# Optimization experiments

Measured on AMD Instinct MI355X. Metric: run time of the kernel, lower is better.

The kernel has to match this reference:

```python
import jax, jax.numpy as jnp
import numpy as np

SEQ, BATCH, IN_DIM, HID = 1024, 512, 128, 128


def _linear_params(key, fan_in, fan_out):
    # matches torch nn.Linear default init: U(-1/sqrt(fan_in), 1/sqrt(fan_in))
    s = 1.0 / np.sqrt(fan_in)
    k1, k2 = jax.random.split(key)
    W = jax.random.uniform(k1, (fan_in, fan_out), minval=-s, maxval=s, dtype=jnp.float32)
    b = jax.random.uniform(k2, (fan_out,), minval=-s, maxval=s, dtype=jnp.float32)
    return W, b


def setup_inputs() -> dict:
    key = jax.random.key(0)
    ks = jax.random.split(key, 5)
    inputs = jax.random.normal(ks[0], (SEQ, BATCH, IN_DIM), dtype=jnp.float32)
    Wf, bf = _linear_params(ks[1], IN_DIM + HID, HID)
    Wi, bi = _linear_params(ks[2], IN_DIM + HID, HID)
    Wg, bg = _linear_params(ks[3], IN_DIM + HID, HID)
    Wo, bo = _linear_params(ks[4], IN_DIM + HID, HID)
    return {"inputs": inputs, "Wf": Wf, "bf": bf, "Wi": Wi, "bi": bi,
            "Wg": Wg, "bg": bg, "Wo": Wo, "bo": bo}


def reference(inputs, Wf, bf, Wi, bi, Wg, bg, Wo, bo):
    # inputs: [seq, batch, in_dim] (time-major, matches torch unbind(dim=0))
    B = inputs.shape[1]
    H = Wf.shape[1]
    h0 = jnp.zeros((B, H), dtype=inputs.dtype)
    c0 = jnp.zeros((B, H), dtype=inputs.dtype)

    def step(carry, x):
        hx, cx = carry
        comb = jnp.concatenate([x, hx], axis=1)  # [B, in_dim+H]
        f_lin = comb @ Wf + bf
        i_lin = comb @ Wi + bi
        g = jnp.tanh(comb @ Wg + bg)
        o = jax.nn.sigmoid(comb @ Wo + bo)
        # Quantum sampler, closed form:
        #  - RX(theta)|0> has <Z> = cos(theta)
        #  - CNOT chain over f-wires pulls Z_j back to Z_0...Z_j -> cumprod of cos
        #  - i-wires untouched by CNOTs -> plain cos
        #  probs = (<Z> + 1) / 2
        f = (jnp.cumprod(jnp.cos(f_lin), axis=1) + 1.0) * 0.5
        i = (jnp.cos(i_lin) + 1.0) * 0.5
        cx_new = f * cx + i * g
        hx_new = o * jnp.tanh(cx_new)
        return (hx_new, cx_new), hx_new

    (hx, cx), outputs = jax.lax.scan(step, (h0, c0), inputs)
    return outputs, hx, cx
```

## Files before the change

kernel.cpp:

```cpp
#include <hip/hip_runtime.h>

#define SEQ   1024
#define BATCH 512
#define HID   128

typedef __attribute__((ext_vector_type(8))) short          short8v;
typedef __attribute__((ext_vector_type(4))) float          float4v;
typedef __attribute__((ext_vector_type(8))) unsigned short ushort8v;

__device__ __forceinline__ unsigned short f2bf(float f) {
    union { float f; unsigned u; } v; v.f = f;
    return (unsigned short)((v.u + 0x7fffu + ((v.u >> 16) & 1u)) >> 16);
}
__device__ __forceinline__ float bf2f(unsigned short u) {
    union { unsigned u; float f; } v; v.u = ((unsigned)u) << 16;
    return v.f;
}
__device__ __forceinline__ unsigned packbf(float a, float b) {
    return (unsigned)f2bf(a) | ((unsigned)f2bf(b) << 16);
}
__device__ __forceinline__ float fast_cos(float x) {
    return __builtin_amdgcn_cosf(x * 0.15915494309189535f);
}
__device__ __forceinline__ float fast_sigmoid(float x) {
    return __builtin_amdgcn_rcpf(1.0f + __builtin_amdgcn_exp2f(-1.4426950408889634f * x));
}
__device__ __forceinline__ float fast_tanh(float x) {
    return 1.0f - 2.0f * __builtin_amdgcn_rcpf(1.0f + __builtin_amdgcn_exp2f(2.8853900817779268f * x));
}
template<int CTRL, int RM>
__device__ __forceinline__ float dpp1(float v) {
    union { float f; int i; } s, o, r;
    s.f = v; o.f = 1.0f;
    r.i = __builtin_amdgcn_update_dpp(o.i, s.i, CTRL, RM, 0xf, false);
    return r.f;
}
#define BAR() do { asm volatile("s_waitcnt lgkmcnt(0)" ::: "memory");  \
                   __builtin_amdgcn_s_barrier();                       \
                   __builtin_amdgcn_sched_barrier(0); } while (0)

__device__ __forceinline__ int zswz(int slot, int g, int c) {
    return slot * 512 + g * 128 + (c ^ ((c >> 5) << 4) ^ ((slot & 2) << 3));
}
__device__ __forceinline__ int gswz(int row, int g, int c) {
    return row * 512 + g * 128 + (c ^ ((c >> 5) << 4));
}

__global__ __launch_bounds__(512, 1) void qlstm_fused(
    const float* __restrict__ X,
    const float* __restrict__ Wf, const float* __restrict__ bfp,
    const float* __restrict__ Wi, const float* __restrict__ bip,
    const float* __restrict__ Wg, const float* __restrict__ bgp,
    const float* __restrict__ Wo, const float* __restrict__ bop,
    float* __restrict__ out)
{
    __shared__ unsigned zr_lds[16 * 4 * 128];
    __shared__ float    ga_lds[2 * 4 * 128];
    __shared__ alignas(8)  unsigned short h_bf[2][HID];
    __shared__ alignas(16) unsigned short x_win[2][16][HID];
    __shared__ float scanT[2];

    const int tid = threadIdx.x, lane = tid & 63, wid = tid >> 6;
    const int l15 = lane & 15, kg = lane >> 4;
    const int b0 = blockIdx.x * 2;
    const int g  = wid >> 1;
    const int hb = wid & 1;
    const int cb = hb * 64;
    const float* Wsel = (g == 0) ? Wf : (g == 1) ? Wi : (g == 2) ? Wg : Wo;
    const float* bsel = (g == 0) ? bfp : (g == 1) ? bip : (g == 2) ? bgp : bop;

    short8v bwh[4][4], bwx[4][4];
    #pragma unroll
    for (int n = 0; n < 4; ++n) {
        const int col = cb + n * 16 + l15;
        #pragma unroll
        for (int ks = 0; ks < 4; ++ks) {
            short8v wh, wx;
            #pragma unroll
            for (int j = 0; j < 8; ++j) {
                const int k = ks * 32 + kg * 8 + j;
                wx[j] = (short)f2bf(Wsel[(size_t)k * HID + col]);
                wh[j] = (short)f2bf(Wsel[(size_t)(128 + k) * HID + col]);
            }
            bwx[n][ks] = wx;
            bwh[n][ks] = wh;
        }
    }
    float biasr[4];
    #pragma unroll
    for (int n = 0; n < 4; ++n) biasr[n] = bsel[cb + n * 16 + l15];

    if (tid < 128) ((unsigned*)h_bf)[tid] = 0u;

    const int crow = wid >> 1;
    const int ccol = (wid & 1) * 64 + lane;
    float c_reg = 0.f, h_last = 0.f;
    const int c_act = cb + lane;

    const int pt  = tid & 255;
    const int sm  = (pt >> 4) & 15;
    const int sbl = pt & 15;
    const size_t xrow_off = ((size_t)(b0 + (sm & 1))) * HID + sbl * 8;
    const int xw_off = (sbl * 16) ^ ((sm & 7) << 4);
    const int xsw = (l15 & 7) << 4;

#define STAGE_XWIN(buf, s0) do {                                                   \
    const float* xp_ = X + ((size_t)((s0) + (sm >> 1)) * BATCH) * HID + xrow_off;  \
    float4v a_ = *(const float4v*)xp_;                                             \
    float4v b_ = *(const float4v*)(xp_ + 4);                                       \
    ushort8v o_;                                                                   \
    o_[0]=f2bf(a_[0]); o_[1]=f2bf(a_[1]); o_[2]=f2bf(a_[2]); o_[3]=f2bf(a_[3]);    \
    o_[4]=f2bf(b_[0]); o_[5]=f2bf(b_[1]); o_[6]=f2bf(b_[2]); o_[7]=f2bf(b_[3]);    \
    *(ushort8v*)((char*)&x_win[buf][sm][0] + xw_off) = o_;                         \
} while (0)

#define LOAD_AX(buf) do {                                                          \
    const char* xb_ = (const char*)&x_win[buf][0][0] + l15 * 256;                  \
    ax[0] = *(const short8v*)(xb_ + ((      kg * 16) ^ xsw));                      \
    ax[1] = *(const short8v*)(xb_ + (( 64 + kg * 16) ^ xsw));                      \
    ax[2] = *(const short8v*)(xb_ + ((128 + kg * 16) ^ xsw));                      \
    ax[3] = *(const short8v*)(xb_ + ((192 + kg * 16) ^ xsw));                      \
} while (0)

#define XTILE(i) do {                                                              \
    float4v xa_;                                                                   \
    xa_[0] = biasr[i]; xa_[1] = biasr[i]; xa_[2] = biasr[i]; xa_[3] = biasr[i];    \
    xa_ = __builtin_amdgcn_mfma_f32_16x16x32_bf16(ax[0], bwx[i][0], xa_, 0, 0, 0); \
    xa_ = __builtin_amdgcn_mfma_f32_16x16x32_bf16(ax[1], bwx[i][1], xa_, 0, 0, 0); \
    xa_ = __builtin_amdgcn_mfma_f32_16x16x32_bf16(ax[2], bwx[i][2], xa_, 0, 0, 0); \
    xa_ = __builtin_amdgcn_mfma_f32_16x16x32_bf16(ax[3], bwx[i][3], xa_, 0, 0, 0); \
    const int se_ = (bnext + kg * 2) & 15;                                         \
    const int cs_ = cb + (i) * 16 + l15;                                           \
    zr_lds[zswz(se_,           g, cs_)] = packbf(xa_[0], xa_[1]);                  \
    zr_lds[zswz((se_ + 1) & 15, g, cs_)] = packbf(xa_[2], xa_[3]);                 \
} while (0)

    short8v ax[4];
    float4v xg0 = {}, xg1 = {};

    if (wid >= 4) { STAGE_XWIN(0, 0); STAGE_XWIN(1, 8); }
    BAR();
    {
        LOAD_AX(0);
        float4v pacc[4];
        #pragma unroll
        for (int n = 0; n < 4; ++n)
            #pragma unroll
            for (int j = 0; j < 4; ++j) pacc[n][j] = biasr[n];
        #pragma unroll
        for (int ks = 0; ks < 4; ++ks)
            #pragma unroll
            for (int n = 0; n < 4; ++n)
                pacc[n] = __builtin_amdgcn_mfma_f32_16x16x32_bf16(ax[ks], bwx[n][ks], pacc[n], 0, 0, 0);
        #pragma unroll
        for (int n = 0; n < 4; ++n) {
            const int se_ = kg * 2;
            const int cs_ = cb + n * 16 + l15;
            zr_lds[zswz(se_,     g, cs_)] = packbf(pacc[n][0], pacc[n][1]);
            zr_lds[zswz(se_ + 1, g, cs_)] = packbf(pacc[n][2], pacc[n][3]);
        }
    }
    BAR();

    #pragma unroll 1
    for (int t = 0; t < SEQ; ++t) {
        const int w = t & 7;
        const int W = t >> 3;
        const int bnext = (t & ~7) + 8;

        const unsigned zp = zr_lds[zswz(t & 15, g, c_act)];
        short8v ah[4];
        #pragma unroll
        for (int ks = 0; ks < 4; ++ks)
            ah[ks] = *(const short8v*)&h_bf[l15 & 1][ks * 32 + kg * 8];

        if (w == 0) {
            if (bnext < SEQ) LOAD_AX((W + 1) & 1);
            if (wid >= 4 && bnext + 8 < SEQ) {
                const float* xp = X + ((size_t)(bnext + 8 + (sm >> 1)) * BATCH) * HID + xrow_off;
                xg0 = *(const float4v*)xp;
                xg1 = *(const float4v*)(xp + 4);
            }
        }

        float4v acc[4];
        #pragma unroll
        for (int n = 0; n < 4; ++n)
            #pragma unroll
            for (int j = 0; j < 4; ++j) acc[n][j] = 0.f;
        __builtin_amdgcn_s_setprio(1);
        #pragma unroll
        for (int ks = 0; ks < 4; ++ks)
            #pragma unroll
            for (int n = 0; n < 4; ++n)
                acc[n] = __builtin_amdgcn_mfma_f32_16x16x32_bf16(ah[ks], bwh[n][ks], acc[n], 0, 0, 0);
        __builtin_amdgcn_s_setprio(0);

        if (bnext < SEQ && (w & 1) == hb) {
            switch (w >> 1) {
                case 0: XTILE(0); break;
                case 1: XTILE(1); break;
                case 2: XTILE(2); break;
                default: XTILE(3); break;
            }
        }

        float s0 = ((kg == 0) ? acc[0][0] : (kg == 1) ? acc[1][0]
                  : (kg == 2) ? acc[2][0] : acc[3][0]) + bf2f((unsigned short)(zp & 0xffffu));
        float s1 = ((kg == 0) ? acc[0][1] : (kg == 1) ? acc[1][1]
                  : (kg == 2) ? acc[2][1] : acc[3][1]) + bf2f((unsigned short)(zp >> 16));

        float v0, v1;
        if (g == 0) {
            float S0 = fast_cos(s0), S1 = fast_cos(s1);
            S0 *= dpp1<0x111, 0xf>(S0);  S1 *= dpp1<0x111, 0xf>(S1);
            S0 *= dpp1<0x112, 0xf>(S0);  S1 *= dpp1<0x112, 0xf>(S1);
            S0 *= dpp1<0x114, 0xf>(S0);  S1 *= dpp1<0x114, 0xf>(S1);
            S0 *= dpp1<0x118, 0xf>(S0);  S1 *= dpp1<0x118, 0xf>(S1);
            const float T00 = __shfl(S0, 15), T01 = __shfl(S0, 31), T02 = __shfl(S0, 47);
            const float T10 = __shfl(S1, 15), T11 = __shfl(S1, 31), T12 = __shfl(S1, 47);
            const float rp0 = (kg == 0) ? 1.f : (kg == 1) ? T00
                            : (kg == 2) ? T00 * T01 : T00 * T01 * T02;
            const float rp1 = (kg == 0) ? 1.f : (kg == 1) ? T10
                            : (kg == 2) ? T10 * T11 : T10 * T11 * T12;
            v0 = rp0 * S0;
            v1 = rp1 * S1;
            if (wid == 0 && lane == 63) { scanT[0] = v0; scanT[1] = v1; }
        } else if (g == 1) {
            v0 = (fast_cos(s0) + 1.f) * .5f;
            v1 = (fast_cos(s1) + 1.f) * .5f;
        } else if (g == 2) {
            v0 = fast_tanh(s0);
            v1 = fast_tanh(s1);
        } else {
            v0 = fast_sigmoid(s0);
            v1 = fast_sigmoid(s1);
        }
        ga_lds[gswz(0, g, c_act)] = v0;
        ga_lds[gswz(1, g, c_act)] = v1;

        BAR();

        if (wid < 4) {
            float fv = ga_lds[gswz(crow, 0, ccol)];
            if (wid & 1) fv *= scanT[crow];
            const float f  = (fv + 1.f) * 0.5f;
            const float iv = ga_lds[gswz(crow, 1, ccol)];
            const float gv = ga_lds[gswz(crow, 2, ccol)];
            const float ov = ga_lds[gswz(crow, 3, ccol)];
            const float cn = fmaf(f, c_reg, iv * gv);
            const float hn = ov * fast_tanh(cn);
            c_reg = cn; h_last = hn;
            h_bf[crow][ccol] = f2bf(hn);
            out[((size_t)t * BATCH + b0 + crow) * HID + ccol] = hn;
        } else if (w == 4 && bnext + 8 < SEQ) {
            ushort8v o_;
            o_[0]=f2bf(xg0[0]); o_[1]=f2bf(xg0[1]); o_[2]=f2bf(xg0[2]); o_[3]=f2bf(xg0[3]);
            o_[4]=f2bf(xg1[0]); o_[5]=f2bf(xg1[1]); o_[6]=f2bf(xg1[2]); o_[7]=f2bf(xg1[3]);
            *(ushort8v*)((char*)&x_win[W & 1][sm][0] + xw_off) = o_;
        }
        BAR();
    }

    if (wid < 4) {
        const size_t base = (size_t)SEQ * BATCH * HID;
        const size_t ro = (size_t)(b0 + crow) * HID + ccol;
        out[base + ro] = h_last;
        out[base + (size_t)BATCH * HID + ro] = c_reg;
    }
#undef STAGE_XWIN
#undef LOAD_AX
#undef XTILE
}

extern "C" void kernel_launch(void* const* d_in, const int* in_sizes, int n_in,
                              void* d_out, int out_size, void* d_ws, size_t ws_size,
                              hipStream_t stream) {
    const float* X  = (const float*)d_in[0];
    const float* Wf = (const float*)d_in[1];
    const float* bf = (const float*)d_in[2];
    const float* Wi = (const float*)d_in[3];
    const float* bi = (const float*)d_in[4];
    const float* Wg = (const float*)d_in[5];
    const float* bg = (const float*)d_in[6];
    const float* Wo = (const float*)d_in[7];
    const float* bo = (const float*)d_in[8];
    float* out = (float*)d_out;
    (void)d_ws; (void)ws_size;

    qlstm_fused<<<BATCH / 2, 512, 0, stream>>>(
        X, Wf, bf, Wi, bi, Wg, bg, Wo, bo, out);
}
```

Before: 1.050 ms.

## Move input-projection weights to LDS and shrink x-window to 4 steps

The input-side weight fragments (bwx) move out of registers into LDS, and the x-projection tiles now read both A and B operands from LDS inside the recurrent loop. The x staging window shrinks from 8 to 4 timesteps per block, so every wave computes one x-tile per step instead of alternating between waves. The aim is to free VGPRs (64 registers of weight fragments) and shorten the per-step register pressure on the serial critical path. The cost is extra LDS reads each step, x-tile work on every wave, and more frequent global prefetches.

```diff
diff --git a/kernel.cpp b/kernel.cpp
--- a/kernel.cpp
+++ b/kernel.cpp
@@ -6,7 +6,7 @@
 
 typedef __attribute__((ext_vector_type(8))) short          short8v;
 typedef __attribute__((ext_vector_type(4))) float          float4v;
-typedef __attribute__((ext_vector_type(8))) unsigned short ushort8v;
+typedef __attribute__((ext_vector_type(4))) unsigned short ushort4v;
 
 __device__ __forceinline__ unsigned short f2bf(float f) {
     union { float f; unsigned u; } v; v.f = f;
@@ -54,10 +54,11 @@
     const float* __restrict__ Wo, const float* __restrict__ bop,
     float* __restrict__ out)
 {
-    __shared__ unsigned zr_lds[16 * 4 * 128];
+    __shared__ short8v  wx_lds[8][4][4][64];
+    __shared__ unsigned zr_lds[8 * 4 * 128];
     __shared__ float    ga_lds[2 * 4 * 128];
     __shared__ alignas(8)  unsigned short h_bf[2][HID];
-    __shared__ alignas(16) unsigned short x_win[2][16][HID];
+    __shared__ alignas(16) unsigned short x_win[2][8][HID];
     __shared__ float scanT[2];
 
     const int tid = threadIdx.x, lane = tid & 63, wid = tid >> 6;
@@ -69,20 +70,30 @@
     const float* Wsel = (g == 0) ? Wf : (g == 1) ? Wi : (g == 2) ? Wg : Wo;
     const float* bsel = (g == 0) ? bfp : (g == 1) ? bip : (g == 2) ? bgp : bop;
 
-    short8v bwh[4][4], bwx[4][4];
     #pragma unroll
     for (int n = 0; n < 4; ++n) {
         const int col = cb + n * 16 + l15;
         #pragma unroll
         for (int ks = 0; ks < 4; ++ks) {
-            short8v wh, wx;
-            #pragma unroll
-            for (int j = 0; j < 8; ++j) {
-                const int k = ks * 32 + kg * 8 + j;
-                wx[j] = (short)f2bf(Wsel[(size_t)k * HID + col]);
-                wh[j] = (short)f2bf(Wsel[(size_t)(128 + k) * HID + col]);
-            }
-            bwx[n][ks] = wx;
+            short8v wx;
+            #pragma unroll
+            for (int j = 0; j < 8; ++j)
+                wx[j] = (short)f2bf(Wsel[(size_t)(ks * 32 + kg * 8 + j) * HID + col]);
+            wx_lds[wid][n][ks][lane] = wx;
+        }
+    }
+    BAR();
+
+    short8v bwh[4][4];
+    #pragma unroll
+    for (int n = 0; n < 4; ++n) {
+        const int col = cb + n * 16 + l15;
+        #pragma unroll
+        for (int ks = 0; ks < 4; ++ks) {
+            short8v wh;
+            #pragma unroll
+            for (int j = 0; j < 8; ++j)
+                wh[j] = (short)f2bf(Wsel[(size_t)(128 + ks * 32 + kg * 8 + j) * HID + col]);
             bwh[n][ks] = wh;
         }
     }
@@ -97,90 +108,60 @@
     float c_reg = 0.f, h_last = 0.f;
     const int c_act = cb + lane;
 
-    const int pt  = tid & 255;
-    const int sm  = (pt >> 4) & 15;
-    const int sbl = pt & 15;
-    const size_t xrow_off = ((size_t)(b0 + (sm & 1))) * HID + sbl * 8;
-    const int xw_off = (sbl * 16) ^ ((sm & 7) << 4);
-    const int xsw = (l15 & 7) << 4;
-
-#define STAGE_XWIN(buf, s0) do {                                                   \
-    const float* xp_ = X + ((size_t)((s0) + (sm >> 1)) * BATCH) * HID + xrow_off;  \
-    float4v a_ = *(const float4v*)xp_;                                             \
-    float4v b_ = *(const float4v*)(xp_ + 4);                                       \
-    ushort8v o_;                                                                   \
-    o_[0]=f2bf(a_[0]); o_[1]=f2bf(a_[1]); o_[2]=f2bf(a_[2]); o_[3]=f2bf(a_[3]);    \
-    o_[4]=f2bf(b_[0]); o_[5]=f2bf(b_[1]); o_[6]=f2bf(b_[2]); o_[7]=f2bf(b_[3]);    \
-    *(ushort8v*)((char*)&x_win[buf][sm][0] + xw_off) = o_;                         \
+    const int pt = tid - 256;
+    const int sm = (pt >> 5) & 7;
+    const int sc = pt & 31;
+    const size_t xrow_off = ((size_t)(b0 + (sm & 1))) * HID + sc * 4;
+    const int xw_boff = sm * 256 + ((((sc >> 1) ^ (sm & 7)) << 4) | ((sc & 1) << 3));
+
+#define STAGE_XWIN(buf, s0) do {                                                    \
+    const float* xp_ = X + ((size_t)((s0) + (sm >> 1)) * BATCH) * HID + xrow_off;   \
+    float4v a_ = *(const float4v*)xp_;                                              \
+    ushort4v o_;                                                                    \
+    o_[0] = f2bf(a_[0]); o_[1] = f2bf(a_[1]); o_[2] = f2bf(a_[2]); o_[3] = f2bf(a_[3]); \
+    *(ushort4v*)((char*)&x_win[buf][0][0] + xw_boff) = o_;                          \
 } while (0)
 
-#define LOAD_AX(buf) do {                                                          \
-    const char* xb_ = (const char*)&x_win[buf][0][0] + l15 * 256;                  \
-    ax[0] = *(const short8v*)(xb_ + ((      kg * 16) ^ xsw));                      \
-    ax[1] = *(const short8v*)(xb_ + (( 64 + kg * 16) ^ xsw));                      \
-    ax[2] = *(const short8v*)(xb_ + ((128 + kg * 16) ^ xsw));                      \
-    ax[3] = *(const short8v*)(xb_ + ((192 + kg * 16) ^ xsw));                      \
+#define XTILE(i, bn, buf) do {                                                      \
+    float4v xa_;                                                                    \
+    xa_[0] = biasr[i]; xa_[1] = biasr[i]; xa_[2] = biasr[i]; xa_[3] = biasr[i];     \
+    _Pragma("unroll")                                                               \
+    for (int ks_ = 0; ks_ < 4; ++ks_) {                                             \
+        short8v axk = *(const short8v*)((const char*)&x_win[buf][0][0] +            \
+            ((l15 & 7) * 256 + (((ks_ * 4 + kg) ^ (l15 & 7)) << 4)));               \
+        xa_ = __builtin_amdgcn_mfma_f32_16x16x32_bf16(axk, wx_lds[wid][i][ks_][lane], xa_, 0, 0, 0); \
+    }                                                                               \
+    if (kg < 2) {                                                                   \
+        const int cs_ = cb + (i) * 16 + l15;                                        \
+        zr_lds[zswz(((bn) + kg * 2) & 7,     g, cs_)] = packbf(xa_[0], xa_[1]);     \
+        zr_lds[zswz(((bn) + kg * 2 + 1) & 7, g, cs_)] = packbf(xa_[2], xa_[3]);     \
+    }                                                                               \
 } while (0)
 
-#define XTILE(i) do {                                                              \
-    float4v xa_;                                                                   \
-    xa_[0] = biasr[i]; xa_[1] = biasr[i]; xa_[2] = biasr[i]; xa_[3] = biasr[i];    \
-    xa_ = __builtin_amdgcn_mfma_f32_16x16x32_bf16(ax[0], bwx[i][0], xa_, 0, 0, 0); \
-    xa_ = __builtin_amdgcn_mfma_f32_16x16x32_bf16(ax[1], bwx[i][1], xa_, 0, 0, 0); \
-    xa_ = __builtin_amdgcn_mfma_f32_16x16x32_bf16(ax[2], bwx[i][2], xa_, 0, 0, 0); \
-    xa_ = __builtin_amdgcn_mfma_f32_16x16x32_bf16(ax[3], bwx[i][3], xa_, 0, 0, 0); \
-    const int se_ = (bnext + kg * 2) & 15;                                         \
-    const int cs_ = cb + (i) * 16 + l15;                                           \
-    zr_lds[zswz(se_,           g, cs_)] = packbf(xa_[0], xa_[1]);                  \
-    zr_lds[zswz((se_ + 1) & 15, g, cs_)] = packbf(xa_[2], xa_[3]);                 \
-} while (0)
-
-    short8v ax[4];
-    float4v xg0 = {}, xg1 = {};
-
-    if (wid >= 4) { STAGE_XWIN(0, 0); STAGE_XWIN(1, 8); }
+    if (wid >= 4) { STAGE_XWIN(0, 0); STAGE_XWIN(1, 4); }
     BAR();
-    {
-        LOAD_AX(0);
-        float4v pacc[4];
-        #pragma unroll
-        for (int n = 0; n < 4; ++n)
-            #pragma unroll
-            for (int j = 0; j < 4; ++j) pacc[n][j] = biasr[n];
-        #pragma unroll
-        for (int ks = 0; ks < 4; ++ks)
-            #pragma unroll
-            for (int n = 0; n < 4; ++n)
-                pacc[n] = __builtin_amdgcn_mfma_f32_16x16x32_bf16(ax[ks], bwx[n][ks], pacc[n], 0, 0, 0);
-        #pragma unroll
-        for (int n = 0; n < 4; ++n) {
-            const int se_ = kg * 2;
-            const int cs_ = cb + n * 16 + l15;
-            zr_lds[zswz(se_,     g, cs_)] = packbf(pacc[n][0], pacc[n][1]);
-            zr_lds[zswz(se_ + 1, g, cs_)] = packbf(pacc[n][2], pacc[n][3]);
-        }
-    }
+    XTILE(0, 0, 0);
+    XTILE(1, 0, 0);
+    XTILE(2, 0, 0);
+    XTILE(3, 0, 0);
     BAR();
+
+    float4v xg = {};
 
     #pragma unroll 1
     for (int t = 0; t < SEQ; ++t) {
-        const int w = t & 7;
-        const int W = t >> 3;
-        const int bnext = (t & ~7) + 8;
-
-        const unsigned zp = zr_lds[zswz(t & 15, g, c_act)];
+        const int w = t & 3;
+        const int W = t >> 2;
+        const int bnext = (t & ~3) + 4;
+
+        const unsigned zp = zr_lds[zswz(t & 7, g, c_act)];
         short8v ah[4];
         #pragma unroll
         for (int ks = 0; ks < 4; ++ks)
             ah[ks] = *(const short8v*)&h_bf[l15 & 1][ks * 32 + kg * 8];
 
-        if (w == 0) {
-            if (bnext < SEQ) LOAD_AX((W + 1) & 1);
-            if (wid >= 4 && bnext + 8 < SEQ) {
-                const float* xp = X + ((size_t)(bnext + 8 + (sm >> 1)) * BATCH) * HID + xrow_off;
-                xg0 = *(const float4v*)xp;
-                xg1 = *(const float4v*)(xp + 4);
-            }
+        if (w == 0 && wid >= 4 && bnext + 4 < SEQ) {
+            xg = *(const float4v*)(X + ((size_t)(bnext + 4 + (sm >> 1)) * BATCH) * HID + xrow_off);
         }
 
         float4v acc[4];
@@ -196,12 +177,13 @@
                 acc[n] = __builtin_amdgcn_mfma_f32_16x16x32_bf16(ah[ks], bwh[n][ks], acc[n], 0, 0, 0);
         __builtin_amdgcn_s_setprio(0);
 
-        if (bnext < SEQ && (w & 1) == hb) {
-            switch (w >> 1) {
-                case 0: XTILE(0); break;
-                case 1: XTILE(1); break;
-                case 2: XTILE(2); break;
-                default: XTILE(3); break;
+        if (bnext < SEQ) {
+            const int xbuf = (W + 1) & 1;
+            switch (w) {
+                case 0: XTILE(0, bnext, xbuf); break;
+                case 1: XTILE(1, bnext, xbuf); break;
+                case 2: XTILE(2, bnext, xbuf); break;
+                default: XTILE(3, bnext, xbuf); break;
             }
         }
 
@@ -253,11 +235,10 @@
             c_reg = cn; h_last = hn;
             h_bf[crow][ccol] = f2bf(hn);
             out[((size_t)t * BATCH + b0 + crow) * HID + ccol] = hn;
-        } else if (w == 4 && bnext + 8 < SEQ) {
-            ushort8v o_;
-            o_[0]=f2bf(xg0[0]); o_[1]=f2bf(xg0[1]); o_[2]=f2bf(xg0[2]); o_[3]=f2bf(xg0[3]);
-            o_[4]=f2bf(xg1[0]); o_[5]=f2bf(xg1[1]); o_[6]=f2bf(xg1[2]); o_[7]=f2bf(xg1[3]);
-            *(ushort8v*)((char*)&x_win[W & 1][sm][0] + xw_off) = o_;
+        } else if (w == 2 && bnext + 4 < SEQ) {
+            ushort4v o_;
+            o_[0] = f2bf(xg[0]); o_[1] = f2bf(xg[1]); o_[2] = f2bf(xg[2]); o_[3] = f2bf(xg[3]);
+            *(ushort4v*)((char*)&x_win[W & 1][0][0] + xw_boff) = o_;
         }
         BAR();
     }
@@ -269,7 +250,6 @@
         out[base + (size_t)BATCH * HID + ro] = c_reg;
     }
 #undef STAGE_XWIN
-#undef LOAD_AX
 #undef XTILE
 }
 
```

After: 1.105 ms. 5.2% more time.
